# Performance work log

Measured on AMD Instinct MI355X. Metric: run time of the kernel, lower is better.

Reference implementation:

```python
import jax, jax.numpy as jnp
import numpy as np

N, E, G = 50000, 800000, 512
IN, HID, H1, H2, OUT = 128, 32, 8, 4, 128
D1, D2 = HID * H1, HID * H2  # 256, 128


def _ln(x, g, b, eps=1e-5):
    m = x.mean(-1, keepdims=True)
    v = jnp.var(x, axis=-1, keepdims=True)
    return (x - m) * jax.lax.rsqrt(v + eps) * g + b


def _gat_conv(x, W, a_src, a_dst, bias, edge_index, heads, ch, concat):
    # PyG GATConv (eval): h = xW per head; e = leakyrelu(a_src.h_src + a_dst.h_dst);
    # segment softmax over destination nodes; scatter-sum messages; self-loops added.
    n = x.shape[0]
    h = (x @ W).reshape(n, heads, ch)                      # [N,H,C]
    asrc = jnp.sum(h * a_src, axis=-1)                     # [N,H]
    adst = jnp.sum(h * a_dst, axis=-1)                     # [N,H]
    loop = jnp.arange(n)
    src = jnp.concatenate([edge_index[0], loop])           # [E+N]
    dst = jnp.concatenate([edge_index[1], loop])
    e = jax.nn.leaky_relu(asrc[src] + adst[dst], 0.2)      # [E+N,H]
    emax = jax.ops.segment_max(e, dst, num_segments=n)
    p = jnp.exp(e - emax[dst])
    denom = jax.ops.segment_sum(p, dst, num_segments=n)
    alpha = p / (denom[dst] + 1e-16)                       # [E+N,H]
    out = jax.ops.segment_sum(h[src] * alpha[..., None], dst, num_segments=n)  # [N,H,C]
    out = out.reshape(n, heads * ch) if concat else out.mean(axis=1)
    return out + bias


def setup_inputs():
    key = jax.random.key(0)
    ks = jax.random.split(key, 32)
    g = lambda i, shape, s=0.05: jax.random.normal(ks[i], shape, dtype=jnp.float32) * s
    inp = {
        "x": jax.random.normal(ks[0], (N, IN), dtype=jnp.float32),
        "edge_index": jax.random.randint(ks[1], (2, E), 0, N, dtype=jnp.int32),
        "batch": jnp.sort(jax.random.randint(ks[2], (N,), 0, G, dtype=jnp.int32)),
        # GAT layer 1: in 128 -> 8 heads x 32
        "W1": g(3, (IN, H1 * HID)), "a_src1": g(4, (H1, HID)), "a_dst1": g(5, (H1, HID)),
        "b1": jnp.zeros((D1,), jnp.float32), "g1": jnp.ones((D1,), jnp.float32), "be1": jnp.zeros((D1,), jnp.float32),
        "pw1": g(6, (IN, D1)), "pb1": jnp.zeros((D1,), jnp.float32),
        # GAT layer 2: 256 -> 4 heads x 32
        "W2": g(7, (D1, H2 * HID)), "a_src2": g(8, (H2, HID)), "a_dst2": g(9, (H2, HID)),
        "b2": jnp.zeros((D2,), jnp.float32), "g2": jnp.ones((D2,), jnp.float32), "be2": jnp.zeros((D2,), jnp.float32),
        "pw2": g(10, (D1, D2)), "pb2": jnp.zeros((D2,), jnp.float32),
        # GAT layer 3: 128 -> 1 head x 128, concat=False
        "W3": g(11, (D2, OUT)), "a_src3": g(12, (1, OUT)), "a_dst3": g(13, (1, OUT)),
        "b3": jnp.zeros((OUT,), jnp.float32), "g3": jnp.ones((OUT,), jnp.float32), "be3": jnp.zeros((OUT,), jnp.float32),
        "pw3": g(14, (D2, OUT)), "pb3": jnp.zeros((OUT,), jnp.float32),
    }
    return inp


def reference(x, edge_index, batch,
              W1, a_src1, a_dst1, b1, g1, be1, pw1, pb1,
              W2, a_src2, a_dst2, b2, g2, be2, pw2, pb2,
              W3, a_src3, a_dst3, b3, g3, be3, pw3, pb3):
    h1 = _gat_conv(x, W1, a_src1, a_dst1, b1, edge_index, H1, HID, True)
    h1 = jax.nn.elu(_ln(h1, g1, be1) + (x @ pw1 + pb1))
    h2 = _gat_conv(h1, W2, a_src2, a_dst2, b2, edge_index, H2, HID, True)
    h2 = jax.nn.elu(_ln(h2, g2, be2) + (h1 @ pw2 + pb2))
    h3 = _gat_conv(h2, W3, a_src3, a_dst3, b3, edge_index, 1, OUT, False)
    h3 = jax.nn.elu(_ln(h3, g3, be3) + (h2 @ pw3 + pb3))
    # jk='last' -> h3; global mean pool per graph
    sums = jax.ops.segment_sum(h3, batch, num_segments=G)              # [G,OUT]
    cnt = jax.ops.segment_sum(jnp.ones((N,), h3.dtype), batch, num_segments=G)
    return sums / jnp.maximum(cnt, 1.0)[:, None]
```

## Files before the change

kernel.cpp:

```cpp
#include <hip/hip_runtime.h>
#include <math.h>


typedef __bf16 bf16x8 __attribute__((ext_vector_type(8)));
typedef float f32x4 __attribute__((ext_vector_type(4)));

static __device__ __forceinline__ float bf2f(unsigned short u) {
  union { unsigned int i; float f; } c;
  c.i = ((unsigned int)u) << 16;
  return c.f;
}
static __device__ __forceinline__ unsigned short f2bf(float f) {
  __bf16 b = (__bf16)f;
  return __builtin_bit_cast(unsigned short, b);
}
static __device__ __forceinline__ float wave_sum(float v) {
#pragma unroll
  for (int off = 1; off < 64; off <<= 1) v += __shfl_xor(v, off, 64);
  return v;
}

template <int K, typename OutT>
__global__ __launch_bounds__(256) void mfma_gemm_kernel(
    const unsigned short* __restrict__ A, const unsigned short* __restrict__ Bp,
    const float* __restrict__ bias, OutT* __restrict__ C, int Ncols) {
  const int lane = threadIdx.x & 63;
  const int w = threadIdx.x >> 6;
  const int ml = lane & 15, kq = lane >> 4;
  const int row0 = blockIdx.y * 64 + (w >> 1) * 32;
  const int colt0 = blockIdx.x * 4 + (w & 1) * 2;
  constexpr int KB = K / 32;

  f32x4 acc00 = {}, acc01 = {}, acc10 = {}, acc11 = {};
  const unsigned short* a0 = A + (size_t)(row0 + ml) * K + kq * 8;
  const unsigned short* b0 = Bp + ((size_t)colt0 * KB * 64 + lane) * 8;
#pragma unroll
  for (int kb = 0; kb < KB; kb++) {
    bf16x8 af0 = __builtin_bit_cast(bf16x8, *(const uint4*)(a0 + kb * 32));
    bf16x8 af1 = __builtin_bit_cast(bf16x8, *(const uint4*)(a0 + 16 * K + kb * 32));
    bf16x8 bf0 = __builtin_bit_cast(bf16x8, *(const uint4*)(b0 + (size_t)kb * 512));
    bf16x8 bf1 = __builtin_bit_cast(bf16x8, *(const uint4*)(b0 + (size_t)(KB + kb) * 512));
    acc00 = __builtin_amdgcn_mfma_f32_16x16x32_bf16(af0, bf0, acc00, 0, 0, 0);
    acc01 = __builtin_amdgcn_mfma_f32_16x16x32_bf16(af0, bf1, acc01, 0, 0, 0);
    acc10 = __builtin_amdgcn_mfma_f32_16x16x32_bf16(af1, bf0, acc10, 0, 0, 0);
    acc11 = __builtin_amdgcn_mfma_f32_16x16x32_bf16(af1, bf1, acc11, 0, 0, 0);
  }
  const int c0 = colt0 * 16 + ml, c1 = c0 + 16;
  float bias0 = 0.f, bias1 = 0.f;
  if (bias) { bias0 = bias[c0]; bias1 = bias[c1]; }
#pragma unroll
  for (int r = 0; r < 4; r++) {
    const size_t rA = (size_t)(row0 + kq * 4 + r);
    const size_t rB = rA + 16;
    float v00 = acc00[r] + bias0, v01 = acc01[r] + bias1;
    float v10 = acc10[r] + bias0, v11 = acc11[r] + bias1;
    if constexpr (sizeof(OutT) == 2) {
      C[rA * Ncols + c0] = f2bf(v00);
      C[rA * Ncols + c1] = f2bf(v01);
      C[rB * Ncols + c0] = f2bf(v10);
      C[rB * Ncols + c1] = f2bf(v11);
    } else {
      C[rA * Ncols + c0] = v00;
      C[rA * Ncols + c1] = v01;
      C[rB * Ncols + c0] = v10;
      C[rB * Ncols + c1] = v11;
    }
  }
}

__global__ void repack_b_kernel(const float* __restrict__ B, unsigned short* __restrict__ Bp,
                                int K, int Ncols) {
  const int idx = blockIdx.x * 256 + threadIdx.x;
  const int KB = K >> 5;
  const int total = (Ncols >> 4) * KB * 64;
  if (idx >= total) return;
  const int lane = idx & 63;
  const int kb = (idx >> 6) % KB;
  const int nt = idx / (KB << 6);
  const int ml = lane & 15, kq = lane >> 4;
  unsigned short* dst = Bp + (size_t)idx * 8;
#pragma unroll
  for (int j = 0; j < 8; j++)
    dst[j] = f2bf(B[(size_t)(kb * 32 + kq * 8 + j) * Ncols + nt * 16 + ml]);
}

__global__ void cast_bf16_kernel(const float* __restrict__ src,
                                 unsigned short* __restrict__ dst, int n4) {
  const int i = blockIdx.x * 256 + threadIdx.x;
  if (i >= n4) return;
  float4 v = ((const float4*)src)[i];
  ushort4 o;
  o.x = f2bf(v.x); o.y = f2bf(v.y); o.z = f2bf(v.z); o.w = f2bf(v.w);
  ((ushort4*)dst)[i] = o;
}

template <int H, int C, int VEC>
__global__ __launch_bounds__(256) void attn_kernel(
    const unsigned short* __restrict__ hfeat, const float* __restrict__ a_src,
    const float* __restrict__ a_dst, float* __restrict__ asrc,
    float* __restrict__ adst, int N) {
  const int DOUT = H * C;
  const int wave = threadIdx.x >> 6;
  const int lane = threadIdx.x & 63;
  const int n = blockIdx.x * 4 + wave;
  if (n >= N) return;

  const unsigned short* hr = &hfeat[(size_t)n * DOUT + lane * VEC];
  float hv[VEC], sv[VEC], dv[VEC];
  if constexpr (VEC == 4) {
    ushort4 t = *(const ushort4*)hr;
    hv[0] = bf2f(t.x); hv[1] = bf2f(t.y); hv[2] = bf2f(t.z); hv[3] = bf2f(t.w);
    float4 s = *(const float4*)&a_src[lane * 4];
    sv[0] = s.x; sv[1] = s.y; sv[2] = s.z; sv[3] = s.w;
    float4 d = *(const float4*)&a_dst[lane * 4];
    dv[0] = d.x; dv[1] = d.y; dv[2] = d.z; dv[3] = d.w;
  } else {
    ushort2 t = *(const ushort2*)hr;
    hv[0] = bf2f(t.x); hv[1] = bf2f(t.y);
    float2 s = *(const float2*)&a_src[lane * 2];
    sv[0] = s.x; sv[1] = s.y;
    float2 d = *(const float2*)&a_dst[lane * 2];
    dv[0] = d.x; dv[1] = d.y;
  }
  float ps = 0.f, pd = 0.f;
#pragma unroll
  for (int i = 0; i < VEC; i++) {
    ps += hv[i] * sv[i];
    pd += hv[i] * dv[i];
  }
  const int L = C / VEC;
#pragma unroll
  for (int off = 1; off < L; off <<= 1) {
    ps += __shfl_xor(ps, off, 64);
    pd += __shfl_xor(pd, off, 64);
  }
  if ((lane % L) == 0) {
    const int hh = lane / L;
    asrc[n * H + hh] = ps;
    adst[n * H + hh] = pd;
  }
}

template <int H, int C, int SPLIT>
__global__ __launch_bounds__(256) void gat_agg_kernel(
    const unsigned short* __restrict__ hfeat, const float* __restrict__ asrc,
    const float* __restrict__ adst, const int* __restrict__ rowptr,
    const int* __restrict__ col, const float* __restrict__ bias,
    const float* __restrict__ gamma, const float* __restrict__ beta,
    const unsigned short* __restrict__ proj, unsigned short* __restrict__ out, int N) {
  constexpr int DOUT = H * C;
  constexpr int RL = DOUT / 4;
  constexpr int PD = 4;
  const int wave = threadIdx.x >> 6;
  const int lane = threadIdx.x & 63;
  const int n = blockIdx.x * 4 + wave;
  if (n >= N) return;
  const int rl = lane % RL;
  const int sub = lane / RL;
  const int myh = (rl * 4) / C;
  const int start = rowptr[n];
  const int deg = rowptr[n + 1] - start;
  const int vlen = deg + 1;
  const float my_adl = adst[n * H + myh];

  float acc0 = 0.f, acc1 = 0.f, acc2 = 0.f, acc3 = 0.f, psum = 0.f;

  for (int chunk = 0; chunk < vlen; chunk += 64) {
    const int loc = chunk + lane;
    const int cv = (loc < deg) ? col[start + loc] : n;
    const int m = min(64, vlen - chunk);
    const int steps = (m + SPLIT - 1) / SPLIT;
    const int ngroups = (steps + PD - 1) / PD;

    float aA[PD], aB[PD];
    ushort4 hA[PD], hB[PD];

#pragma unroll
    for (int k = 0; k < PD; k++) {
      const int local = k * SPLIT + sub;
      int s = __shfl(cv, local & 63);
      if (local >= m) s = n;
      aA[k] = asrc[s * H + myh];
      hA[k] = *(const ushort4*)&hfeat[(size_t)s * DOUT + rl * 4];
    }
    for (int g = 0; g < ngroups; g += 2) {
      if (g + 1 < ngroups) {
#pragma unroll
        for (int k = 0; k < PD; k++) {
          const int local = ((g + 1) * PD + k) * SPLIT + sub;
          int s = __shfl(cv, local & 63);
          if (local >= m) s = n;
          aB[k] = asrc[s * H + myh];
          hB[k] = *(const ushort4*)&hfeat[(size_t)s * DOUT + rl * 4];
        }
      }
#pragma unroll
      for (int k = 0; k < PD; k++) {
        const int local = (g * PD + k) * SPLIT + sub;
        float e = aA[k] + my_adl;
        e = (e > 0.f) ? e : 0.2f * e;
        float p = __expf(e);
        p = (local < m) ? p : 0.f;
        psum += p;
        acc0 += bf2f(hA[k].x) * p;
        acc1 += bf2f(hA[k].y) * p;
        acc2 += bf2f(hA[k].z) * p;
        acc3 += bf2f(hA[k].w) * p;
      }
      if (g + 1 < ngroups) {
        if (g + 2 < ngroups) {
#pragma unroll
          for (int k = 0; k < PD; k++) {
            const int local = ((g + 2) * PD + k) * SPLIT + sub;
            int s = __shfl(cv, local & 63);
            if (local >= m) s = n;
            aA[k] = asrc[s * H + myh];
            hA[k] = *(const ushort4*)&hfeat[(size_t)s * DOUT + rl * 4];
          }
        }
#pragma unroll
        for (int k = 0; k < PD; k++) {
          const int local = ((g + 1) * PD + k) * SPLIT + sub;
          float e = aB[k] + my_adl;
          e = (e > 0.f) ? e : 0.2f * e;
          float p = __expf(e);
          p = (local < m) ? p : 0.f;
          psum += p;
          acc0 += bf2f(hB[k].x) * p;
          acc1 += bf2f(hB[k].y) * p;
          acc2 += bf2f(hB[k].z) * p;
          acc3 += bf2f(hB[k].w) * p;
        }
      }
    }
  }

  if constexpr (SPLIT == 2) {
    psum += __shfl_xor(psum, 32);
    acc0 += __shfl_xor(acc0, 32);
    acc1 += __shfl_xor(acc1, 32);
    acc2 += __shfl_xor(acc2, 32);
    acc3 += __shfl_xor(acc3, 32);
  }

  const float rs = 1.f / (psum + 1e-16f);
  const int c0 = rl * 4;
  const float4 bi = *(const float4*)&bias[c0];
  float v0 = acc0 * rs + bi.x;
  float v1 = acc1 * rs + bi.y;
  float v2 = acc2 * rs + bi.z;
  float v3 = acc3 * rs + bi.w;

  const float mean = wave_sum(v0 + v1 + v2 + v3) / (float)(DOUT * SPLIT);
  const float d0 = v0 - mean, d1 = v1 - mean, d2 = v2 - mean, d3 = v3 - mean;
  const float var = wave_sum(d0 * d0 + d1 * d1 + d2 * d2 + d3 * d3) / (float)(DOUT * SPLIT);
  const float rstd = rsqrtf(var + 1e-5f);

  const float4 ga = *(const float4*)&gamma[c0];
  const float4 be = *(const float4*)&beta[c0];
  const ushort4 pr = *(const ushort4*)&proj[(size_t)n * DOUT + c0];
  float o0 = d0 * rstd * ga.x + be.x + bf2f(pr.x);
  float o1 = d1 * rstd * ga.y + be.y + bf2f(pr.y);
  float o2 = d2 * rstd * ga.z + be.z + bf2f(pr.z);
  float o3 = d3 * rstd * ga.w + be.w + bf2f(pr.w);
  o0 = (o0 > 0.f) ? o0 : expm1f(o0);
  o1 = (o1 > 0.f) ? o1 : expm1f(o1);
  o2 = (o2 > 0.f) ? o2 : expm1f(o2);
  o3 = (o3 > 0.f) ? o3 : expm1f(o3);
  if (sub == 0) {
    ushort4 ov;
    ov.x = f2bf(o0); ov.y = f2bf(o1); ov.z = f2bf(o2); ov.w = f2bf(o3);
    *(ushort4*)&out[(size_t)n * DOUT + c0] = ov;
  }
}

__global__ void hist_kernel(const int* __restrict__ dst, int* __restrict__ cnt, int E) {
  const int e = blockIdx.x * 256 + threadIdx.x;
  if (e < E) atomicAdd(&cnt[dst[e]], 1);
}

__global__ __launch_bounds__(256) void scan1_kernel(int* __restrict__ cnt,
                                                    int* __restrict__ sums, int N) {
  __shared__ int sm[256];
  const int i = blockIdx.x * 256 + threadIdx.x;
  const int v = (i < N) ? cnt[i] : 0;
  sm[threadIdx.x] = v;
  __syncthreads();
  for (int off = 1; off < 256; off <<= 1) {
    const int t = (threadIdx.x >= off) ? sm[threadIdx.x - off] : 0;
    __syncthreads();
    sm[threadIdx.x] += t;
    __syncthreads();
  }
  if (i < N) cnt[i] = sm[threadIdx.x] - v;
  if (threadIdx.x == 255) sums[blockIdx.x] = sm[255];
}

__global__ __launch_bounds__(256) void scan2_kernel(int* __restrict__ sums, int nb) {
  __shared__ int sm[256];
  const int v = (threadIdx.x < nb) ? sums[threadIdx.x] : 0;
  sm[threadIdx.x] = v;
  __syncthreads();
  for (int off = 1; off < 256; off <<= 1) {
    const int t = (threadIdx.x >= off) ? sm[threadIdx.x - off] : 0;
    __syncthreads();
    sm[threadIdx.x] += t;
    __syncthreads();
  }
  if (threadIdx.x < nb) sums[threadIdx.x] = sm[threadIdx.x] - v;
}

__global__ void scan3_kernel(const int* __restrict__ cnt, const int* __restrict__ sums,
                             int* __restrict__ rowptr, int* __restrict__ cursor,
                             int N, int E) {
  const int i = blockIdx.x * 256 + threadIdx.x;
  if (i < N) {
    const int r = cnt[i] + sums[blockIdx.x];
    rowptr[i] = r;
    cursor[i] = r;
  }
  if (i == 0) rowptr[N] = E;
}

__global__ void scatter_kernel(const int* __restrict__ src, const int* __restrict__ dst,
                               int* __restrict__ cursor, int* __restrict__ col, int E) {
  const int e = blockIdx.x * 256 + threadIdx.x;
  if (e < E) {
    const int p = atomicAdd(&cursor[dst[e]], 1);
    col[p] = src[e];
  }
}

__global__ __launch_bounds__(128) void pool_kernel(const unsigned short* __restrict__ h3,
                                                   const int* __restrict__ batch,
                                                   float* __restrict__ out, int N) {
  __shared__ int sse[2];
  const int g = blockIdx.x;
  if (threadIdx.x == 0) {
    int lo = 0, hi = N;
    while (lo < hi) { const int mid = (lo + hi) >> 1; if (batch[mid] < g) lo = mid + 1; else hi = mid; }
    sse[0] = lo;
    lo = 0; hi = N;
    while (lo < hi) { const int mid = (lo + hi) >> 1; if (batch[mid] < g + 1) lo = mid + 1; else hi = mid; }
    sse[1] = lo;
  }
  __syncthreads();
  const int s = sse[0], e = sse[1];
  float sum = 0.f;
  for (int r = s; r < e; r++) sum += bf2f(h3[(size_t)r * 128 + threadIdx.x]);
  out[g * 128 + threadIdx.x] = (e > s) ? sum / (float)(e - s) : 0.f;
}

extern "C" void kernel_launch(void* const* d_in, const int* in_sizes, int n_in,
                              void* d_out, int out_size, void* d_ws, size_t ws_size,
                              hipStream_t stream) {
  const float* x      = (const float*)d_in[0];
  const int* edge_idx = (const int*)d_in[1];
  const int* batch    = (const int*)d_in[2];
  const float* W1     = (const float*)d_in[3];
  const float* a_src1 = (const float*)d_in[4];
  const float* a_dst1 = (const float*)d_in[5];
  const float* b1     = (const float*)d_in[6];
  const float* g1     = (const float*)d_in[7];
  const float* be1    = (const float*)d_in[8];
  const float* pw1    = (const float*)d_in[9];
  const float* pb1    = (const float*)d_in[10];
  const float* W2     = (const float*)d_in[11];
  const float* a_src2 = (const float*)d_in[12];
  const float* a_dst2 = (const float*)d_in[13];
  const float* b2     = (const float*)d_in[14];
  const float* g2     = (const float*)d_in[15];
  const float* be2    = (const float*)d_in[16];
  const float* pw2    = (const float*)d_in[17];
  const float* pb2    = (const float*)d_in[18];
  const float* W3     = (const float*)d_in[19];
  const float* a_src3 = (const float*)d_in[20];
  const float* a_dst3 = (const float*)d_in[21];
  const float* b3     = (const float*)d_in[22];
  const float* g3     = (const float*)d_in[23];
  const float* be3    = (const float*)d_in[24];
  const float* pw3    = (const float*)d_in[25];
  const float* pb3    = (const float*)d_in[26];

  const int NN = in_sizes[0] / 128;
  const int E  = in_sizes[1] / 2;
  const int G  = out_size / 128;
  const int M64 = (NN + 63) & ~63;

  size_t off = 0;
  auto alloc = [&](size_t bytes) {
    size_t r = off;
    off += (bytes + 255) & ~(size_t)255;
    return r;
  };
  char* ws = (char*)d_ws;
  unsigned short* big0 = (unsigned short*)(ws + alloc((size_t)M64 * 256 * 2));
  unsigned short* big1 = (unsigned short*)(ws + alloc((size_t)M64 * 256 * 2));
  unsigned short* s0   = (unsigned short*)(ws + alloc((size_t)M64 * 128 * 2));
  unsigned short* s1   = (unsigned short*)(ws + alloc((size_t)M64 * 128 * 2));
  unsigned short* projb = (unsigned short*)(ws + alloc((size_t)M64 * 256 * 2));
  float* asrcB = (float*)(ws + alloc((size_t)NN * 8 * 4));
  float* adstB = (float*)(ws + alloc((size_t)NN * 8 * 4));
  int* rowptr  = (int*)(ws + alloc((size_t)(NN + 1) * 4));
  int* cnt     = (int*)(ws + alloc((size_t)NN * 4));
  int* cursor  = (int*)(ws + alloc((size_t)NN * 4));
  int* colb    = (int*)(ws + alloc((size_t)E * 4));
  int* sums    = (int*)(ws + alloc(256 * 4));
  unsigned short* BpW1 = (unsigned short*)(ws + alloc(128 * 256 * 2));
  unsigned short* BpP1 = (unsigned short*)(ws + alloc(128 * 256 * 2));
  unsigned short* BpW2 = (unsigned short*)(ws + alloc(256 * 128 * 2));
  unsigned short* BpP2 = (unsigned short*)(ws + alloc(256 * 128 * 2));
  unsigned short* BpW3 = (unsigned short*)(ws + alloc(128 * 128 * 2));
  unsigned short* BpP3 = (unsigned short*)(ws + alloc(128 * 128 * 2));
  (void)ws_size; (void)n_in;

  const int EB = (E + 255) / 256;
  const int NB = (NN + 255) / 256;
  const int NW = (NN + 3) / 4;
  const int MB = M64 / 64;
  const int pad = M64 - NN;

  hipMemsetAsync(cnt, 0, (size_t)NN * 4, stream);
  hist_kernel<<<EB, 256, 0, stream>>>(edge_idx + E, cnt, E);
  scan1_kernel<<<NB, 256, 0, stream>>>(cnt, sums, NN);
  scan2_kernel<<<1, 256, 0, stream>>>(sums, NB);
  scan3_kernel<<<NB, 256, 0, stream>>>(cnt, sums, rowptr, cursor, NN, E);
  scatter_kernel<<<EB, 256, 0, stream>>>(edge_idx, edge_idx + E, cursor, colb, E);

  cast_bf16_kernel<<<(NN * 128 / 4 + 255) / 256, 256, 0, stream>>>(x, s0, NN * 128 / 4);
  if (pad) {
    hipMemsetAsync(s0 + (size_t)NN * 128, 0, (size_t)pad * 128 * 2, stream);
    hipMemsetAsync(big1 + (size_t)NN * 256, 0, (size_t)pad * 256 * 2, stream);
    hipMemsetAsync(s1 + (size_t)NN * 128, 0, (size_t)pad * 128 * 2, stream);
  }

  repack_b_kernel<<<((256 / 16) * (128 / 32) * 64 + 255) / 256, 256, 0, stream>>>(W1, BpW1, 128, 256);
  repack_b_kernel<<<((256 / 16) * (128 / 32) * 64 + 255) / 256, 256, 0, stream>>>(pw1, BpP1, 128, 256);
  repack_b_kernel<<<((128 / 16) * (256 / 32) * 64 + 255) / 256, 256, 0, stream>>>(W2, BpW2, 256, 128);
  repack_b_kernel<<<((128 / 16) * (256 / 32) * 64 + 255) / 256, 256, 0, stream>>>(pw2, BpP2, 256, 128);
  repack_b_kernel<<<((128 / 16) * (128 / 32) * 64 + 255) / 256, 256, 0, stream>>>(W3, BpW3, 128, 128);
  repack_b_kernel<<<((128 / 16) * (128 / 32) * 64 + 255) / 256, 256, 0, stream>>>(pw3, BpP3, 128, 128);

  mfma_gemm_kernel<128, unsigned short><<<dim3(4, MB), 256, 0, stream>>>(s0, BpW1, nullptr, big0, 256);
  mfma_gemm_kernel<128, unsigned short><<<dim3(4, MB), 256, 0, stream>>>(s0, BpP1, pb1, projb, 256);
  attn_kernel<8, 32, 4><<<NW, 256, 0, stream>>>(big0, a_src1, a_dst1, asrcB, adstB, NN);
  gat_agg_kernel<8, 32, 1><<<NW, 256, 0, stream>>>(big0, asrcB, adstB, rowptr, colb, b1, g1, be1, projb, big1, NN);

  mfma_gemm_kernel<256, unsigned short><<<dim3(2, MB), 256, 0, stream>>>(big1, BpW2, nullptr, s0, 128);
  mfma_gemm_kernel<256, unsigned short><<<dim3(2, MB), 256, 0, stream>>>(big1, BpP2, pb2, projb, 128);
  attn_kernel<4, 32, 2><<<NW, 256, 0, stream>>>(s0, a_src2, a_dst2, asrcB, adstB, NN);
  gat_agg_kernel<4, 32, 2><<<NW, 256, 0, stream>>>(s0, asrcB, adstB, rowptr, colb, b2, g2, be2, projb, s1, NN);

  mfma_gemm_kernel<128, unsigned short><<<dim3(2, MB), 256, 0, stream>>>(s1, BpW3, nullptr, big0, 128);
  mfma_gemm_kernel<128, unsigned short><<<dim3(2, MB), 256, 0, stream>>>(s1, BpP3, pb3, projb, 128);
  attn_kernel<1, 128, 2><<<NW, 256, 0, stream>>>(big0, a_src3, a_dst3, asrcB, adstB, NN);
  gat_agg_kernel<1, 128, 2><<<NW, 256, 0, stream>>>(big0, asrcB, adstB, rowptr, colb, b3, g3, be3, projb, s0, NN);

  pool_kernel<<<G, 128, 0, stream>>>(s0, batch, (float*)d_out, NN);
}
```

Measured before the change: 559.2 us.

## Fuse paired GEMMs sharing input and widen aggregation loads to 8 bf16

Merges the feature GEMM and the residual projection GEMM, which read the same activation, into one kernel so the A tiles are loaded once and one launch per layer is removed. The aggregation kernel now has each lane handle 8 channels through 16-byte gathers instead of 8-byte ones, and SPLIT doubles so more neighbors are processed in parallel per wave. A generalized cross-lane reduction combines the partial sums. The fused GEMM keeps eight accumulators per wave, which raises register pressure.

Result: faster. 544.8 us (-2.6%).

```diff
diff --git a/kernel.cpp b/kernel.cpp
--- a/kernel.cpp
+++ b/kernel.cpp
@@ -19,11 +19,22 @@
   for (int off = 1; off < 64; off <<= 1) v += __shfl_xor(v, off, 64);
   return v;
 }
-
-template <int K, typename OutT>
-__global__ __launch_bounds__(256) void mfma_gemm_kernel(
-    const unsigned short* __restrict__ A, const unsigned short* __restrict__ Bp,
-    const float* __restrict__ bias, OutT* __restrict__ C, int Ncols) {
+static __device__ __forceinline__ float bflo(unsigned int w) {
+  union { unsigned int i; float f; } c;
+  c.i = w << 16;
+  return c.f;
+}
+static __device__ __forceinline__ float bfhi(unsigned int w) {
+  union { unsigned int i; float f; } c;
+  c.i = w & 0xFFFF0000u;
+  return c.f;
+}
+
+template <int K>
+__global__ __launch_bounds__(256) void fused_gemm_kernel(
+    const unsigned short* __restrict__ A, const unsigned short* __restrict__ Bp1,
+    const unsigned short* __restrict__ Bp2, const float* __restrict__ bias2,
+    unsigned short* __restrict__ C1, unsigned short* __restrict__ C2, int Ncols) {
   const int lane = threadIdx.x & 63;
   const int w = threadIdx.x >> 6;
   const int ml = lane & 15, kq = lane >> 4;
@@ -31,40 +42,42 @@
   const int colt0 = blockIdx.x * 4 + (w & 1) * 2;
   constexpr int KB = K / 32;
 
-  f32x4 acc00 = {}, acc01 = {}, acc10 = {}, acc11 = {};
+  f32x4 w00 = {}, w01 = {}, w10 = {}, w11 = {};
+  f32x4 p00 = {}, p01 = {}, p10 = {}, p11 = {};
   const unsigned short* a0 = A + (size_t)(row0 + ml) * K + kq * 8;
-  const unsigned short* b0 = Bp + ((size_t)colt0 * KB * 64 + lane) * 8;
+  const unsigned short* b1 = Bp1 + ((size_t)colt0 * KB * 64 + lane) * 8;
+  const unsigned short* b2 = Bp2 + ((size_t)colt0 * KB * 64 + lane) * 8;
 #pragma unroll
   for (int kb = 0; kb < KB; kb++) {
     bf16x8 af0 = __builtin_bit_cast(bf16x8, *(const uint4*)(a0 + kb * 32));
     bf16x8 af1 = __builtin_bit_cast(bf16x8, *(const uint4*)(a0 + 16 * K + kb * 32));
-    bf16x8 bf0 = __builtin_bit_cast(bf16x8, *(const uint4*)(b0 + (size_t)kb * 512));
-    bf16x8 bf1 = __builtin_bit_cast(bf16x8, *(const uint4*)(b0 + (size_t)(KB + kb) * 512));
-    acc00 = __builtin_amdgcn_mfma_f32_16x16x32_bf16(af0, bf0, acc00, 0, 0, 0);
-    acc01 = __builtin_amdgcn_mfma_f32_16x16x32_bf16(af0, bf1, acc01, 0, 0, 0);
-    acc10 = __builtin_amdgcn_mfma_f32_16x16x32_bf16(af1, bf0, acc10, 0, 0, 0);
-    acc11 = __builtin_amdgcn_mfma_f32_16x16x32_bf16(af1, bf1, acc11, 0, 0, 0);
+    bf16x8 bw0 = __builtin_bit_cast(bf16x8, *(const uint4*)(b1 + (size_t)kb * 512));
+    bf16x8 bw1 = __builtin_bit_cast(bf16x8, *(const uint4*)(b1 + (size_t)(KB + kb) * 512));
+    bf16x8 bp0 = __builtin_bit_cast(bf16x8, *(const uint4*)(b2 + (size_t)kb * 512));
+    bf16x8 bp1 = __builtin_bit_cast(bf16x8, *(const uint4*)(b2 + (size_t)(KB + kb) * 512));
+    w00 = __builtin_amdgcn_mfma_f32_16x16x32_bf16(af0, bw0, w00, 0, 0, 0);
+    w01 = __builtin_amdgcn_mfma_f32_16x16x32_bf16(af0, bw1, w01, 0, 0, 0);
+    w10 = __builtin_amdgcn_mfma_f32_16x16x32_bf16(af1, bw0, w10, 0, 0, 0);
+    w11 = __builtin_amdgcn_mfma_f32_16x16x32_bf16(af1, bw1, w11, 0, 0, 0);
+    p00 = __builtin_amdgcn_mfma_f32_16x16x32_bf16(af0, bp0, p00, 0, 0, 0);
+    p01 = __builtin_amdgcn_mfma_f32_16x16x32_bf16(af0, bp1, p01, 0, 0, 0);
+    p10 = __builtin_amdgcn_mfma_f32_16x16x32_bf16(af1, bp0, p10, 0, 0, 0);
+    p11 = __builtin_amdgcn_mfma_f32_16x16x32_bf16(af1, bp1, p11, 0, 0, 0);
   }
   const int c0 = colt0 * 16 + ml, c1 = c0 + 16;
-  float bias0 = 0.f, bias1 = 0.f;
-  if (bias) { bias0 = bias[c0]; bias1 = bias[c1]; }
+  const float bi0 = bias2[c0], bi1 = bias2[c1];
 #pragma unroll
   for (int r = 0; r < 4; r++) {
     const size_t rA = (size_t)(row0 + kq * 4 + r);
     const size_t rB = rA + 16;
-    float v00 = acc00[r] + bias0, v01 = acc01[r] + bias1;
-    float v10 = acc10[r] + bias0, v11 = acc11[r] + bias1;
-    if constexpr (sizeof(OutT) == 2) {
-      C[rA * Ncols + c0] = f2bf(v00);
-      C[rA * Ncols + c1] = f2bf(v01);
-      C[rB * Ncols + c0] = f2bf(v10);
-      C[rB * Ncols + c1] = f2bf(v11);
-    } else {
-      C[rA * Ncols + c0] = v00;
-      C[rA * Ncols + c1] = v01;
-      C[rB * Ncols + c0] = v10;
-      C[rB * Ncols + c1] = v11;
-    }
+    C1[rA * Ncols + c0] = f2bf(w00[r]);
+    C1[rA * Ncols + c1] = f2bf(w01[r]);
+    C1[rB * Ncols + c0] = f2bf(w10[r]);
+    C1[rB * Ncols + c1] = f2bf(w11[r]);
+    C2[rA * Ncols + c0] = f2bf(p00[r] + bi0);
+    C2[rA * Ncols + c1] = f2bf(p01[r] + bi1);
+    C2[rB * Ncols + c0] = f2bf(p10[r] + bi0);
+    C2[rB * Ncols + c1] = f2bf(p11[r] + bi1);
   }
 }
 
@@ -149,7 +162,7 @@
     const float* __restrict__ gamma, const float* __restrict__ beta,
     const unsigned short* __restrict__ proj, unsigned short* __restrict__ out, int N) {
   constexpr int DOUT = H * C;
-  constexpr int RL = DOUT / 4;
+  constexpr int RL = DOUT / 8;
   constexpr int PD = 4;
   const int wave = threadIdx.x >> 6;
   const int lane = threadIdx.x & 63;
@@ -157,13 +170,17 @@
   if (n >= N) return;
   const int rl = lane % RL;
   const int sub = lane / RL;
-  const int myh = (rl * 4) / C;
+  const int c0 = rl * 8;
+  const int myh = c0 / C;
   const int start = rowptr[n];
   const int deg = rowptr[n + 1] - start;
   const int vlen = deg + 1;
   const float my_adl = adst[n * H + myh];
 
-  float acc0 = 0.f, acc1 = 0.f, acc2 = 0.f, acc3 = 0.f, psum = 0.f;
+  float acc[8];
+#pragma unroll
+  for (int i = 0; i < 8; i++) acc[i] = 0.f;
+  float psum = 0.f;
 
   for (int chunk = 0; chunk < vlen; chunk += 64) {
     const int loc = chunk + lane;
@@ -173,7 +190,7 @@
     const int ngroups = (steps + PD - 1) / PD;
 
     float aA[PD], aB[PD];
-    ushort4 hA[PD], hB[PD];
+    uint4 hA[PD], hB[PD];
 
 #pragma unroll
     for (int k = 0; k < PD; k++) {
@@ -181,7 +198,7 @@
       int s = __shfl(cv, local & 63);
       if (local >= m) s = n;
       aA[k] = asrc[s * H + myh];
-      hA[k] = *(const ushort4*)&hfeat[(size_t)s * DOUT + rl * 4];
+      hA[k] = *(const uint4*)&hfeat[(size_t)s * DOUT + c0];
     }
     for (int g = 0; g < ngroups; g += 2) {
       if (g + 1 < ngroups) {
@@ -191,7 +208,7 @@
           int s = __shfl(cv, local & 63);
           if (local >= m) s = n;
           aB[k] = asrc[s * H + myh];
-          hB[k] = *(const ushort4*)&hfeat[(size_t)s * DOUT + rl * 4];
+          hB[k] = *(const uint4*)&hfeat[(size_t)s * DOUT + c0];
         }
       }
 #pragma unroll
@@ -202,10 +219,10 @@
         float p = __expf(e);
         p = (local < m) ? p : 0.f;
         psum += p;
-        acc0 += bf2f(hA[k].x) * p;
-        acc1 += bf2f(hA[k].y) * p;
-        acc2 += bf2f(hA[k].z) * p;
-        acc3 += bf2f(hA[k].w) * p;
+        acc[0] += bflo(hA[k].x) * p; acc[1] += bfhi(hA[k].x) * p;
+        acc[2] += bflo(hA[k].y) * p; acc[3] += bfhi(hA[k].y) * p;
+        acc[4] += bflo(hA[k].z) * p; acc[5] += bfhi(hA[k].z) * p;
+        acc[6] += bflo(hA[k].w) * p; acc[7] += bfhi(hA[k].w) * p;
       }
       if (g + 1 < ngroups) {
         if (g + 2 < ngroups) {
@@ -215,7 +232,7 @@
             int s = __shfl(cv, local & 63);
             if (local >= m) s = n;
             aA[k] = asrc[s * H + myh];
-            hA[k] = *(const ushort4*)&hfeat[(size_t)s * DOUT + rl * 4];
+            hA[k] = *(const uint4*)&hfeat[(size_t)s * DOUT + c0];
           }
         }
 #pragma unroll
@@ -226,51 +243,72 @@
           float p = __expf(e);
           p = (local < m) ? p : 0.f;
           psum += p;
-          acc0 += bf2f(hB[k].x) * p;
-          acc1 += bf2f(hB[k].y) * p;
-          acc2 += bf2f(hB[k].z) * p;
-          acc3 += bf2f(hB[k].w) * p;
+          acc[0] += bflo(hB[k].x) * p; acc[1] += bfhi(hB[k].x) * p;
+          acc[2] += bflo(hB[k].y) * p; acc[3] += bfhi(hB[k].y) * p;
+          acc[4] += bflo(hB[k].z) * p; acc[5] += bfhi(hB[k].z) * p;
+          acc[6] += bflo(hB[k].w) * p; acc[7] += bfhi(hB[k].w) * p;
         }
       }
     }
   }
 
-  if constexpr (SPLIT == 2) {
-    psum += __shfl_xor(psum, 32);
-    acc0 += __shfl_xor(acc0, 32);
-    acc1 += __shfl_xor(acc1, 32);
-    acc2 += __shfl_xor(acc2, 32);
-    acc3 += __shfl_xor(acc3, 32);
+#pragma unroll
+  for (int o = RL; o < 64; o <<= 1) {
+    psum += __shfl_xor(psum, o);
+#pragma unroll
+    for (int i = 0; i < 8; i++) acc[i] += __shfl_xor(acc[i], o);
   }
 
   const float rs = 1.f / (psum + 1e-16f);
-  const int c0 = rl * 4;
-  const float4 bi = *(const float4*)&bias[c0];
-  float v0 = acc0 * rs + bi.x;
-  float v1 = acc1 * rs + bi.y;
-  float v2 = acc2 * rs + bi.z;
-  float v3 = acc3 * rs + bi.w;
-
-  const float mean = wave_sum(v0 + v1 + v2 + v3) / (float)(DOUT * SPLIT);
-  const float d0 = v0 - mean, d1 = v1 - mean, d2 = v2 - mean, d3 = v3 - mean;
-  const float var = wave_sum(d0 * d0 + d1 * d1 + d2 * d2 + d3 * d3) / (float)(DOUT * SPLIT);
+  const float4 bi0 = *(const float4*)&bias[c0];
+  const float4 bi1 = *(const float4*)&bias[c0 + 4];
+  float v[8];
+  v[0] = acc[0] * rs + bi0.x; v[1] = acc[1] * rs + bi0.y;
+  v[2] = acc[2] * rs + bi0.z; v[3] = acc[3] * rs + bi0.w;
+  v[4] = acc[4] * rs + bi1.x; v[5] = acc[5] * rs + bi1.y;
+  v[6] = acc[6] * rs + bi1.z; v[7] = acc[7] * rs + bi1.w;
+
+  float s8 = 0.f;
+#pragma unroll
+  for (int i = 0; i < 8; i++) s8 += v[i];
+  const float mean = wave_sum(s8) / (float)(DOUT * SPLIT);
+  float q8 = 0.f;
+#pragma unroll
+  for (int i = 0; i < 8; i++) {
+    v[i] -= mean;
+    q8 += v[i] * v[i];
+  }
+  const float var = wave_sum(q8) / (float)(DOUT * SPLIT);
   const float rstd = rsqrtf(var + 1e-5f);
 
-  const float4 ga = *(const float4*)&gamma[c0];
-  const float4 be = *(const float4*)&beta[c0];
-  const ushort4 pr = *(const ushort4*)&proj[(size_t)n * DOUT + c0];
-  float o0 = d0 * rstd * ga.x + be.x + bf2f(pr.x);
-  float o1 = d1 * rstd * ga.y + be.y + bf2f(pr.y);
-  float o2 = d2 * rstd * ga.z + be.z + bf2f(pr.z);
-  float o3 = d3 * rstd * ga.w + be.w + bf2f(pr.w);
+  const float4 ga0 = *(const float4*)&gamma[c0];
+  const float4 ga1 = *(const float4*)&gamma[c0 + 4];
+  const float4 be0 = *(const float4*)&beta[c0];
+  const float4 be1 = *(const float4*)&beta[c0 + 4];
+  const uint4 pr = *(const uint4*)&proj[(size_t)n * DOUT + c0];
+  float o0 = v[0] * rstd * ga0.x + be0.x + bflo(pr.x);
+  float o1 = v[1] * rstd * ga0.y + be0.y + bfhi(pr.x);
+  float o2 = v[2] * rstd * ga0.z + be0.z + bflo(pr.y);
+  float o3 = v[3] * rstd * ga0.w + be0.w + bfhi(pr.y);
+  float o4 = v[4] * rstd * ga1.x + be1.x + bflo(pr.z);
+  float o5 = v[5] * rstd * ga1.y + be1.y + bfhi(pr.z);
+  float o6 = v[6] * rstd * ga1.z + be1.z + bflo(pr.w);
+  float o7 = v[7] * rstd * ga1.w + be1.w + bfhi(pr.w);
   o0 = (o0 > 0.f) ? o0 : expm1f(o0);
   o1 = (o1 > 0.f) ? o1 : expm1f(o1);
   o2 = (o2 > 0.f) ? o2 : expm1f(o2);
   o3 = (o3 > 0.f) ? o3 : expm1f(o3);
+  o4 = (o4 > 0.f) ? o4 : expm1f(o4);
+  o5 = (o5 > 0.f) ? o5 : expm1f(o5);
+  o6 = (o6 > 0.f) ? o6 : expm1f(o6);
+  o7 = (o7 > 0.f) ? o7 : expm1f(o7);
   if (sub == 0) {
-    ushort4 ov;
-    ov.x = f2bf(o0); ov.y = f2bf(o1); ov.z = f2bf(o2); ov.w = f2bf(o3);
-    *(ushort4*)&out[(size_t)n * DOUT + c0] = ov;
+    uint4 ov;
+    ov.x = (unsigned int)f2bf(o0) | ((unsigned int)f2bf(o1) << 16);
+    ov.y = (unsigned int)f2bf(o2) | ((unsigned int)f2bf(o3) << 16);
+    ov.z = (unsigned int)f2bf(o4) | ((unsigned int)f2bf(o5) << 16);
+    ov.w = (unsigned int)f2bf(o6) | ((unsigned int)f2bf(o7) << 16);
+    *(uint4*)&out[(size_t)n * DOUT + c0] = ov;
   }
 }
 
@@ -441,20 +479,17 @@
   repack_b_kernel<<<((128 / 16) * (128 / 32) * 64 + 255) / 256, 256, 0, stream>>>(W3, BpW3, 128, 128);
   repack_b_kernel<<<((128 / 16) * (128 / 32) * 64 + 255) / 256, 256, 0, stream>>>(pw3, BpP3, 128, 128);
 
-  mfma_gemm_kernel<128, unsigned short><<<dim3(4, MB), 256, 0, stream>>>(s0, BpW1, nullptr, big0, 256);
-  mfma_gemm_kernel<128, unsigned short><<<dim3(4, MB), 256, 0, stream>>>(s0, BpP1, pb1, projb, 256);
+  fused_gemm_kernel<128><<<dim3(4, MB), 256, 0, stream>>>(s0, BpW1, BpP1, pb1, big0, projb, 256);
   attn_kernel<8, 32, 4><<<NW, 256, 0, stream>>>(big0, a_src1, a_dst1, asrcB, adstB, NN);
-  gat_agg_kernel<8, 32, 1><<<NW, 256, 0, stream>>>(big0, asrcB, adstB, rowptr, colb, b1, g1, be1, projb, big1, NN);
-
-  mfma_gemm_kernel<256, unsigned short><<<dim3(2, MB), 256, 0, stream>>>(big1, BpW2, nullptr, s0, 128);
-  mfma_gemm_kernel<256, unsigned short><<<dim3(2, MB), 256, 0, stream>>>(big1, BpP2, pb2, projb, 128);
+  gat_agg_kernel<8, 32, 2><<<NW, 256, 0, stream>>>(big0, asrcB, adstB, rowptr, colb, b1, g1, be1, projb, big1, NN);
+
+  fused_gemm_kernel<256><<<dim3(2, MB), 256, 0, stream>>>(big1, BpW2, BpP2, pb2, s0, projb, 128);
   attn_kernel<4, 32, 2><<<NW, 256, 0, stream>>>(s0, a_src2, a_dst2, asrcB, adstB, NN);
-  gat_agg_kernel<4, 32, 2><<<NW, 256, 0, stream>>>(s0, asrcB, adstB, rowptr, colb, b2, g2, be2, projb, s1, NN);
-
-  mfma_gemm_kernel<128, unsigned short><<<dim3(2, MB), 256, 0, stream>>>(s1, BpW3, nullptr, big0, 128);
-  mfma_gemm_kernel<128, unsigned short><<<dim3(2, MB), 256, 0, stream>>>(s1, BpP3, pb3, projb, 128);
+  gat_agg_kernel<4, 32, 4><<<NW, 256, 0, stream>>>(s0, asrcB, adstB, rowptr, colb, b2, g2, be2, projb, s1, NN);
+
+  fused_gemm_kernel<128><<<dim3(2, MB), 256, 0, stream>>>(s1, BpW3, BpP3, pb3, big0, projb, 128);
   attn_kernel<1, 128, 2><<<NW, 256, 0, stream>>>(big0, a_src3, a_dst3, asrcB, adstB, NN);
-  gat_agg_kernel<1, 128, 2><<<NW, 256, 0, stream>>>(big0, asrcB, adstB, rowptr, colb, b3, g3, be3, projb, s0, NN);
+  gat_agg_kernel<1, 128, 4><<<NW, 256, 0, stream>>>(big0, asrcB, adstB, rowptr, colb, b3, g3, be3, projb, s0, NN);
 
   pool_kernel<<<G, 128, 0, stream>>>(s0, batch, (float*)d_out, NN);
 }
```
